# Optimization experiments

Hardware: AMD Instinct MI355X
Metric: run time of the kernel (lower is better)

Reference implementation:

```python
import jax, jax.numpy as jnp
import numpy as np

# Graph sampling geometry (2-layer neighbor sampling, fanouts 16 and 10)
N0 = 1_048_576   # layer-0 src nodes (full frontier, features supplied)
N1 = 65_536      # layer-0 dst nodes == layer-1 src nodes
N2 = 4_096       # layer-1 dst nodes (seeds)
DEG0, DEG1 = 16, 10
E0, E1 = N1 * DEG0, N2 * DEG1
D_IN, D_H, D_OUT = 128, 256, 47


def _init_linear(key, out_f, in_f):
    s = 1.0 / np.sqrt(in_f)
    return jax.random.uniform(key, (out_f, in_f), jnp.float32, -s, s)


def setup_inputs() -> dict:
    key = jax.random.key(0)
    ks = jax.random.split(key, 10)
    x = jax.random.normal(ks[0], (N0, D_IN), dtype=jnp.float32)
    # CSC: indptr over dst nodes (uniform degree), indices = src node ids
    indptr0 = jnp.arange(N1 + 1, dtype=jnp.int32) * DEG0
    indices0 = jax.random.randint(ks[1], (E0,), 0, N0, dtype=jnp.int32)
    indptr1 = jnp.arange(N2 + 1, dtype=jnp.int32) * DEG1
    indices1 = jax.random.randint(ks[2], (E1,), 0, N1, dtype=jnp.int32)
    return {
        "x": x,
        "indices0": indices0, "indptr0": indptr0,
        "indices1": indices1, "indptr1": indptr1,
        "Wl0": _init_linear(ks[3], D_H, D_IN), "bl0": jnp.zeros((D_H,), jnp.float32),
        "Wr0": _init_linear(ks[4], D_H, D_IN),
        "Wl1": _init_linear(ks[5], D_H, D_H), "bl1": jnp.zeros((D_H,), jnp.float32),
        "Wr1": _init_linear(ks[6], D_H, D_H),
        "Wo": _init_linear(ks[7], D_OUT, D_H), "bo": jnp.zeros((D_OUT,), jnp.float32),
    }


def expand_indptr(indptr, num_edges):
    # gb.expand_indptr: edge e -> dst j with indptr[j] <= e < indptr[j+1]
    e = jnp.arange(num_edges, dtype=indptr.dtype)
    return jnp.searchsorted(indptr, e, side="right") - 1


def sage_conv(h, src, dst, dst_size, Wl, bl, Wr):
    # PyG SAGEConv (mean aggr): lin_l(mean_{neighbors}) + lin_r(x_dst)
    msg = h[src]                                                    # [E, d]
    summed = jax.ops.segment_sum(msg, dst, num_segments=dst_size)  # [dst, d]
    cnt = jax.ops.segment_sum(jnp.ones_like(dst, dtype=h.dtype), dst,
                              num_segments=dst_size)
    mean = summed / jnp.maximum(cnt, 1.0)[:, None]
    return mean @ Wl.T + bl + h[:dst_size] @ Wr.T


def reference(x, indices0, indptr0, indices1, indptr1,
              Wl0, bl0, Wr0, Wl1, bl1, Wr1, Wo, bo):
    # layer 0
    dst0 = expand_indptr(indptr0, E0)
    h = sage_conv(x, indices0, dst0, N1, Wl0, bl0, Wr0)
    h = jax.nn.gelu(h, approximate=False)  # dropout p=0.0 -> identity
    # layer 1
    dst1 = expand_indptr(indptr1, E1)
    h = sage_conv(h, indices1, dst1, N2, Wl1, bl1, Wr1)
    h = jax.nn.gelu(h, approximate=False)
    # final projection
    return h @ Wo.T + bo
```

## Files before the change

kernel.cpp:

```cpp
#include <hip/hip_runtime.h>
#include <math.h>

#define N0 1048576
#define N1 65536
#define N2 4096
#define DEG0 16
#define DEG1 10
#define D_IN 128
#define D_H 256
#define D_OUT 47

__device__ __forceinline__ float gelu_exact(float x) {
    return 0.5f * x * (1.0f + erff(x * 0.70710678118654752f));
}

template <int DEG, int F4>
__global__ __launch_bounds__(256) void agg_mean_kernel(
    const float4* __restrict__ feat, const int* __restrict__ idx,
    float4* __restrict__ out, int ndst)
{
    const int lane  = threadIdx.x % F4;
    const int local = threadIdx.x / F4;
    const int per_block = 256 / F4;
    const int j = blockIdx.x * per_block + local;
    if (j >= ndst) return;

    const int* ip = idx + (long)j * DEG;
    int srcs[DEG];
#pragma unroll
    for (int e = 0; e < DEG; ++e) srcs[e] = ip[e];

    float4 acc = make_float4(0.f, 0.f, 0.f, 0.f);
#pragma unroll
    for (int e = 0; e < DEG; ++e) {
        float4 v = feat[(long)srcs[e] * F4 + lane];
        acc.x += v.x; acc.y += v.y; acc.z += v.z; acc.w += v.w;
    }
    const float r = 1.0f / (float)DEG;
    acc.x *= r; acc.y *= r; acc.z *= r; acc.w *= r;
    out[(long)j * F4 + lane] = acc;
}

template <int K1, int K2>
__global__ __launch_bounds__(256) void gemm_gelu_kernel(
    const float* __restrict__ A1, const float* __restrict__ A2,
    const float* __restrict__ B1, const float* __restrict__ B2,
    const float* __restrict__ bias, float* __restrict__ C, int M)
{
    constexpr int BM = 128, BN = 64, BK = 32;
    __shared__ float As[BK][BM + 4];
    __shared__ float Bs[BK][BN + 4];

    const int tid = threadIdx.x;
    const int bm = blockIdx.x, bn = blockIdx.y;
    const int tx = tid & 15;
    const int ty = tid >> 4;
    const int r  = tid >> 3;
    const int c4 = (tid & 7) * 4;

    float acc[8][4];
#pragma unroll
    for (int i = 0; i < 8; ++i)
#pragma unroll
        for (int j = 0; j < 4; ++j) acc[i][j] = 0.f;

    constexpr int KT = (K1 + K2) / BK;
#pragma unroll 1
    for (int kt = 0; kt < KT; ++kt) {
        const int k0 = kt * BK;
        const float* Asrc; const float* Bsrc; int koff;
        if (k0 < K1) { Asrc = A1; Bsrc = B1; koff = k0; }
        else         { Asrc = A2; Bsrc = B2; koff = k0 - K1; }
        const int lda = (k0 < K1) ? K1 : K2;

#pragma unroll
        for (int rr = 0; rr < 4; ++rr) {
            const int row = r + rr * 32;
            float4 v = *(const float4*)(Asrc + (long)(bm * BM + row) * lda + koff + c4);
            As[c4 + 0][row] = v.x; As[c4 + 1][row] = v.y;
            As[c4 + 2][row] = v.z; As[c4 + 3][row] = v.w;
        }
#pragma unroll
        for (int nn = 0; nn < 2; ++nn) {
            const int n = r + nn * 32;
            float4 v = *(const float4*)(Bsrc + (long)(bn * BN + n) * lda + koff + c4);
            Bs[c4 + 0][n] = v.x; Bs[c4 + 1][n] = v.y;
            Bs[c4 + 2][n] = v.z; Bs[c4 + 3][n] = v.w;
        }
        __syncthreads();

#pragma unroll
        for (int k = 0; k < BK; ++k) {
            float4 a0 = *(const float4*)&As[k][ty * 8];
            float4 a1 = *(const float4*)&As[k][ty * 8 + 4];
            float4 b  = *(const float4*)&Bs[k][tx * 4];
            const float av[8] = {a0.x, a0.y, a0.z, a0.w, a1.x, a1.y, a1.z, a1.w};
            const float bv[4] = {b.x, b.y, b.z, b.w};
#pragma unroll
            for (int i = 0; i < 8; ++i)
#pragma unroll
                for (int j = 0; j < 4; ++j)
                    acc[i][j] += av[i] * bv[j];
        }
        __syncthreads();
    }

    float4 b4 = *(const float4*)(bias + bn * BN + tx * 4);
    const float bb[4] = {b4.x, b4.y, b4.z, b4.w};
#pragma unroll
    for (int i = 0; i < 8; ++i) {
        const int row = bm * BM + ty * 8 + i;
        float4 o;
        o.x = gelu_exact(acc[i][0] + bb[0]);
        o.y = gelu_exact(acc[i][1] + bb[1]);
        o.z = gelu_exact(acc[i][2] + bb[2]);
        o.w = gelu_exact(acc[i][3] + bb[3]);
        *(float4*)(C + (long)row * D_H + bn * BN + tx * 4) = o;
    }
}

__global__ __launch_bounds__(64) void proj_kernel(
    const float* __restrict__ H, const float* __restrict__ Wo,
    const float* __restrict__ bo, float* __restrict__ out)
{
    __shared__ float hrow[D_H];
    const int i = blockIdx.x;
    ((float4*)hrow)[threadIdx.x] = ((const float4*)(H + (long)i * D_H))[threadIdx.x];
    __syncthreads();
    const int n = threadIdx.x;
    if (n < D_OUT) {
        const float* w = Wo + (long)n * D_H;
        float s = 0.f;
#pragma unroll 8
        for (int k = 0; k < D_H; ++k) s += hrow[k] * w[k];
        out[(long)i * D_OUT + n] = s + bo[n];
    }
}

extern "C" void kernel_launch(void* const* d_in, const int* in_sizes, int n_in,
                              void* d_out, int out_size, void* d_ws, size_t ws_size,
                              hipStream_t stream)
{
    const float* x        = (const float*)d_in[0];
    const int*   indices0 = (const int*)d_in[1];
    const int*   indices1 = (const int*)d_in[3];
    const float* Wl0 = (const float*)d_in[5];
    const float* bl0 = (const float*)d_in[6];
    const float* Wr0 = (const float*)d_in[7];
    const float* Wl1 = (const float*)d_in[8];
    const float* bl1 = (const float*)d_in[9];
    const float* Wr1 = (const float*)d_in[10];
    const float* Wo  = (const float*)d_in[11];
    const float* bo  = (const float*)d_in[12];
    float* out = (float*)d_out;

    float* mean0 = (float*)d_ws;
    float* h0    = mean0 + (size_t)N1 * D_IN;
    float* mean1 = h0    + (size_t)N1 * D_H;
    float* h1    = mean1 + (size_t)N2 * D_H;

    agg_mean_kernel<DEG0, D_IN / 4><<<N1 / (256 / (D_IN / 4)), 256, 0, stream>>>(
        (const float4*)x, indices0, (float4*)mean0, N1);

    gemm_gelu_kernel<D_IN, D_IN><<<dim3(N1 / 128, D_H / 64), 256, 0, stream>>>(
        mean0, x, Wl0, Wr0, bl0, h0, N1);

    agg_mean_kernel<DEG1, D_H / 4><<<N2 / (256 / (D_H / 4)), 256, 0, stream>>>(
        (const float4*)h0, indices1, (float4*)mean1, N2);

    gemm_gelu_kernel<D_H, D_H><<<dim3(N2 / 128, D_H / 64), 256, 0, stream>>>(
        mean1, h0, Wl1, Wr1, bl1, h1, N2);

    proj_kernel<<<N2, 64, 0, stream>>>(h1, Wo, bo, out);
}
```

Before: 869.9 us.

## Fuse aggregation with GEMM and use split-bf16 MFMA for all layers

Replaces the separate mean-aggregation and fp32 SIMT GEMM kernels with fused per-layer kernels. Each fused kernel gathers neighbor rows into registers, splits them into hi/lo bf16 pairs and runs three MFMA 16x16x32 bf16 products to keep near-fp32 accuracy. Intermediate activations are stored as bf16 hi/lo pairs, and weights are pre-split by a small prep kernel on every call. This removes the mean buffer round trips and the slow FP32 FMA GEMM. The cost is triple MFMA work and weight fragments read straight from global memory without LDS staging.

```diff
diff --git a/kernel.cpp b/kernel.cpp
--- a/kernel.cpp
+++ b/kernel.cpp
@@ -10,130 +10,311 @@
 #define D_H 256
 #define D_OUT 47
 
+typedef unsigned int uint32;
+typedef __attribute__((ext_vector_type(8))) short bf16x8;
+typedef __attribute__((ext_vector_type(4))) float f32x4;
+
+__device__ __forceinline__ unsigned short f2b(float x) {
+    uint32 u = __float_as_uint(x);
+    return (unsigned short)((u + 0x7fffu + ((u >> 16) & 1u)) >> 16);
+}
+__device__ __forceinline__ float b2f(unsigned short h) {
+    return __uint_as_float(((uint32)h) << 16);
+}
 __device__ __forceinline__ float gelu_exact(float x) {
     return 0.5f * x * (1.0f + erff(x * 0.70710678118654752f));
 }
-
-template <int DEG, int F4>
-__global__ __launch_bounds__(256) void agg_mean_kernel(
-    const float4* __restrict__ feat, const int* __restrict__ idx,
-    float4* __restrict__ out, int ndst)
-{
-    const int lane  = threadIdx.x % F4;
-    const int local = threadIdx.x / F4;
-    const int per_block = 256 / F4;
-    const int j = blockIdx.x * per_block + local;
-    if (j >= ndst) return;
-
-    const int* ip = idx + (long)j * DEG;
-    int srcs[DEG];
-#pragma unroll
-    for (int e = 0; e < DEG; ++e) srcs[e] = ip[e];
-
-    float4 acc = make_float4(0.f, 0.f, 0.f, 0.f);
-#pragma unroll
-    for (int e = 0; e < DEG; ++e) {
-        float4 v = feat[(long)srcs[e] * F4 + lane];
-        acc.x += v.x; acc.y += v.y; acc.z += v.z; acc.w += v.w;
-    }
-    const float r = 1.0f / (float)DEG;
-    acc.x *= r; acc.y *= r; acc.z *= r; acc.w *= r;
-    out[(long)j * F4 + lane] = acc;
-}
-
-template <int K1, int K2>
-__global__ __launch_bounds__(256) void gemm_gelu_kernel(
-    const float* __restrict__ A1, const float* __restrict__ A2,
-    const float* __restrict__ B1, const float* __restrict__ B2,
-    const float* __restrict__ bias, float* __restrict__ C, int M)
-{
-    constexpr int BM = 128, BN = 64, BK = 32;
-    __shared__ float As[BK][BM + 4];
-    __shared__ float Bs[BK][BN + 4];
-
-    const int tid = threadIdx.x;
-    const int bm = blockIdx.x, bn = blockIdx.y;
-    const int tx = tid & 15;
-    const int ty = tid >> 4;
-    const int r  = tid >> 3;
-    const int c4 = (tid & 7) * 4;
-
-    float acc[8][4];
-#pragma unroll
-    for (int i = 0; i < 8; ++i)
-#pragma unroll
-        for (int j = 0; j < 4; ++j) acc[i][j] = 0.f;
-
-    constexpr int KT = (K1 + K2) / BK;
-#pragma unroll 1
-    for (int kt = 0; kt < KT; ++kt) {
-        const int k0 = kt * BK;
-        const float* Asrc; const float* Bsrc; int koff;
-        if (k0 < K1) { Asrc = A1; Bsrc = B1; koff = k0; }
-        else         { Asrc = A2; Bsrc = B2; koff = k0 - K1; }
-        const int lda = (k0 < K1) ? K1 : K2;
-
-#pragma unroll
-        for (int rr = 0; rr < 4; ++rr) {
-            const int row = r + rr * 32;
-            float4 v = *(const float4*)(Asrc + (long)(bm * BM + row) * lda + koff + c4);
-            As[c4 + 0][row] = v.x; As[c4 + 1][row] = v.y;
-            As[c4 + 2][row] = v.z; As[c4 + 3][row] = v.w;
-        }
-#pragma unroll
-        for (int nn = 0; nn < 2; ++nn) {
-            const int n = r + nn * 32;
-            float4 v = *(const float4*)(Bsrc + (long)(bn * BN + n) * lda + koff + c4);
-            Bs[c4 + 0][n] = v.x; Bs[c4 + 1][n] = v.y;
-            Bs[c4 + 2][n] = v.z; Bs[c4 + 3][n] = v.w;
-        }
-        __syncthreads();
-
-#pragma unroll
-        for (int k = 0; k < BK; ++k) {
-            float4 a0 = *(const float4*)&As[k][ty * 8];
-            float4 a1 = *(const float4*)&As[k][ty * 8 + 4];
-            float4 b  = *(const float4*)&Bs[k][tx * 4];
-            const float av[8] = {a0.x, a0.y, a0.z, a0.w, a1.x, a1.y, a1.z, a1.w};
-            const float bv[4] = {b.x, b.y, b.z, b.w};
-#pragma unroll
-            for (int i = 0; i < 8; ++i)
-#pragma unroll
-                for (int j = 0; j < 4; ++j)
-                    acc[i][j] += av[i] * bv[j];
-        }
-        __syncthreads();
-    }
-
-    float4 b4 = *(const float4*)(bias + bn * BN + tx * 4);
-    const float bb[4] = {b4.x, b4.y, b4.z, b4.w};
-#pragma unroll
-    for (int i = 0; i < 8; ++i) {
-        const int row = bm * BM + ty * 8 + i;
-        float4 o;
-        o.x = gelu_exact(acc[i][0] + bb[0]);
-        o.y = gelu_exact(acc[i][1] + bb[1]);
-        o.z = gelu_exact(acc[i][2] + bb[2]);
-        o.w = gelu_exact(acc[i][3] + bb[3]);
-        *(float4*)(C + (long)row * D_H + bn * BN + tx * 4) = o;
-    }
-}
-
-__global__ __launch_bounds__(64) void proj_kernel(
-    const float* __restrict__ H, const float* __restrict__ Wo,
+__device__ __forceinline__ void split8(float4 a, float4 b, bf16x8& fh, bf16x8& fl) {
+    float t[8] = {a.x, a.y, a.z, a.w, b.x, b.y, b.z, b.w};
+#pragma unroll
+    for (int j = 0; j < 8; ++j) {
+        unsigned short h = f2b(t[j]);
+        fh[j] = (short)h;
+        fl[j] = (short)f2b(t[j] - b2f(h));
+    }
+}
+
+__global__ __launch_bounds__(256) void prep_weights(
+    const float4* __restrict__ Wl0, const float4* __restrict__ Wr0,
+    const float4* __restrict__ Wl1, const float4* __restrict__ Wr1,
+    const float4* __restrict__ Wo,
+    ushort4* __restrict__ wl0h, ushort4* __restrict__ wl0l,
+    ushort4* __restrict__ wr0h, ushort4* __restrict__ wr0l,
+    ushort4* __restrict__ wl1h, ushort4* __restrict__ wl1l,
+    ushort4* __restrict__ wr1h, ushort4* __restrict__ wr1l,
+    ushort4* __restrict__ woh,  ushort4* __restrict__ wol)
+{
+    const int b = blockIdx.x, t = threadIdx.x;
+    const float4* src; ushort4 *dh, *dl; int i, n4;
+    if (b < 32)       { src = Wl0; dh = wl0h; dl = wl0l; i = b * 256 + t;         n4 = 8192;  }
+    else if (b < 64)  { src = Wr0; dh = wr0h; dl = wr0l; i = (b - 32) * 256 + t;  n4 = 8192;  }
+    else if (b < 128) { src = Wl1; dh = wl1h; dl = wl1l; i = (b - 64) * 256 + t;  n4 = 16384; }
+    else if (b < 192) { src = Wr1; dh = wr1h; dl = wr1l; i = (b - 128) * 256 + t; n4 = 16384; }
+    else              { src = Wo;  dh = woh;  dl = wol;  i = (b - 192) * 256 + t; n4 = 3008;  }
+    if (i < n4) {
+        float4 v = src[i];
+        ushort4 h, l;
+        h.x = f2b(v.x); l.x = f2b(v.x - b2f(h.x));
+        h.y = f2b(v.y); l.y = f2b(v.y - b2f(h.y));
+        h.z = f2b(v.z); l.z = f2b(v.z - b2f(h.z));
+        h.w = f2b(v.w); l.w = f2b(v.w - b2f(h.w));
+        dh[i] = h; dl[i] = l;
+    }
+}
+
+__global__ __launch_bounds__(256) void layer0_fused(
+    const float* __restrict__ x, const int* __restrict__ idx,
+    const unsigned short* __restrict__ Blh, const unsigned short* __restrict__ Bll,
+    const unsigned short* __restrict__ Brh, const unsigned short* __restrict__ Brl,
+    const float* __restrict__ bias,
+    unsigned short* __restrict__ oh, unsigned short* __restrict__ ol)
+{
+    const int tid  = threadIdx.x;
+    const int w    = tid >> 6;
+    const int lane = tid & 63;
+    const int quad = lane >> 4;
+    const int l16  = lane & 15;
+    const int m    = blockIdx.x * 64 + w * 16 + l16;
+
+    float mean[4][8];
+#pragma unroll
+    for (int c = 0; c < 4; ++c)
+#pragma unroll
+        for (int j = 0; j < 8; ++j) mean[c][j] = 0.f;
+
+    int srcs[DEG0];
+    {
+        const int4* ip = (const int4*)(idx + (size_t)m * DEG0);
+#pragma unroll
+        for (int q = 0; q < 4; ++q) {
+            int4 v = ip[q];
+            srcs[4 * q + 0] = v.x; srcs[4 * q + 1] = v.y;
+            srcs[4 * q + 2] = v.z; srcs[4 * q + 3] = v.w;
+        }
+    }
+#pragma unroll
+    for (int e = 0; e < DEG0; ++e) {
+        const float* row = x + (size_t)srcs[e] * D_IN + quad * 8;
+#pragma unroll
+        for (int c = 0; c < 4; ++c) {
+            float4 v0 = *(const float4*)(row + c * 32);
+            float4 v1 = *(const float4*)(row + c * 32 + 4);
+            mean[c][0] += v0.x; mean[c][1] += v0.y; mean[c][2] += v0.z; mean[c][3] += v0.w;
+            mean[c][4] += v1.x; mean[c][5] += v1.y; mean[c][6] += v1.z; mean[c][7] += v1.w;
+        }
+    }
+    bf16x8 a1h[4], a1l[4];
+#pragma unroll
+    for (int c = 0; c < 4; ++c)
+#pragma unroll
+        for (int j = 0; j < 8; ++j) {
+            float v = mean[c][j] * 0.0625f;
+            unsigned short h = f2b(v);
+            a1h[c][j] = (short)h;
+            a1l[c][j] = (short)f2b(v - b2f(h));
+        }
+
+    f32x4 acc[16];
+#pragma unroll
+    for (int nt = 0; nt < 16; ++nt) acc[nt] = (f32x4)0.f;
+
+#pragma unroll
+    for (int c = 0; c < 4; ++c) {
+        const int ko = c * 32 + quad * 8;
+#pragma unroll
+        for (int nt = 0; nt < 16; ++nt) {
+            const size_t bo_ = (size_t)(nt * 16 + l16) * D_IN + ko;
+            bf16x8 bh = *(const bf16x8*)(Blh + bo_);
+            bf16x8 bl = *(const bf16x8*)(Bll + bo_);
+            acc[nt] = __builtin_amdgcn_mfma_f32_16x16x32_bf16(a1l[c], bh, acc[nt], 0, 0, 0);
+            acc[nt] = __builtin_amdgcn_mfma_f32_16x16x32_bf16(a1h[c], bl, acc[nt], 0, 0, 0);
+            acc[nt] = __builtin_amdgcn_mfma_f32_16x16x32_bf16(a1h[c], bh, acc[nt], 0, 0, 0);
+        }
+    }
+    const float* xrow = x + (size_t)m * D_IN + quad * 8;
+#pragma unroll
+    for (int c = 0; c < 4; ++c) {
+        float4 v0 = *(const float4*)(xrow + c * 32);
+        float4 v1 = *(const float4*)(xrow + c * 32 + 4);
+        bf16x8 ah, al;
+        split8(v0, v1, ah, al);
+        const int ko = c * 32 + quad * 8;
+#pragma unroll
+        for (int nt = 0; nt < 16; ++nt) {
+            const size_t bo_ = (size_t)(nt * 16 + l16) * D_IN + ko;
+            bf16x8 bh = *(const bf16x8*)(Brh + bo_);
+            bf16x8 bl = *(const bf16x8*)(Brl + bo_);
+            acc[nt] = __builtin_amdgcn_mfma_f32_16x16x32_bf16(al, bh, acc[nt], 0, 0, 0);
+            acc[nt] = __builtin_amdgcn_mfma_f32_16x16x32_bf16(ah, bl, acc[nt], 0, 0, 0);
+            acc[nt] = __builtin_amdgcn_mfma_f32_16x16x32_bf16(ah, bh, acc[nt], 0, 0, 0);
+        }
+    }
+
+    const int row0 = blockIdx.x * 64 + w * 16 + quad * 4;
+#pragma unroll
+    for (int nt = 0; nt < 16; ++nt) {
+        const int col = nt * 16 + l16;
+        const float bb = bias[col];
+#pragma unroll
+        for (int r = 0; r < 4; ++r) {
+            float v = gelu_exact(acc[nt][r] + bb);
+            unsigned short h = f2b(v);
+            const size_t o = (size_t)(row0 + r) * D_H + col;
+            oh[o] = h;
+            ol[o] = f2b(v - b2f(h));
+        }
+    }
+}
+
+__global__ __launch_bounds__(128) void layer1_fused(
+    const unsigned short* __restrict__ fh, const unsigned short* __restrict__ fl,
+    const int* __restrict__ idx,
+    const unsigned short* __restrict__ Blh, const unsigned short* __restrict__ Bll,
+    const unsigned short* __restrict__ Brh, const unsigned short* __restrict__ Brl,
+    const float* __restrict__ bias,
+    unsigned short* __restrict__ oh, unsigned short* __restrict__ ol)
+{
+    const int tid  = threadIdx.x;
+    const int w    = tid >> 6;
+    const int lane = tid & 63;
+    const int quad = lane >> 4;
+    const int l16  = lane & 15;
+    const int m    = blockIdx.x * 32 + w * 16 + l16;
+
+    float mean[8][8];
+#pragma unroll
+    for (int c = 0; c < 8; ++c)
+#pragma unroll
+        for (int j = 0; j < 8; ++j) mean[c][j] = 0.f;
+
+    int srcs[DEG1];
+#pragma unroll
+    for (int e = 0; e < DEG1; ++e) srcs[e] = idx[(size_t)m * DEG1 + e];
+
+#pragma unroll
+    for (int e = 0; e < DEG1; ++e) {
+        const unsigned short* rh = fh + (size_t)srcs[e] * D_H + quad * 8;
+        const unsigned short* rl = fl + (size_t)srcs[e] * D_H + quad * 8;
+#pragma unroll
+        for (int c = 0; c < 8; ++c) {
+            bf16x8 hv = *(const bf16x8*)(rh + c * 32);
+            bf16x8 lv = *(const bf16x8*)(rl + c * 32);
+#pragma unroll
+            for (int j = 0; j < 8; ++j)
+                mean[c][j] += b2f((unsigned short)hv[j]) + b2f((unsigned short)lv[j]);
+        }
+    }
+    bf16x8 a1h[8], a1l[8];
+#pragma unroll
+    for (int c = 0; c < 8; ++c)
+#pragma unroll
+        for (int j = 0; j < 8; ++j) {
+            float v = mean[c][j] * 0.1f;
+            unsigned short h = f2b(v);
+            a1h[c][j] = (short)h;
+            a1l[c][j] = (short)f2b(v - b2f(h));
+        }
+
+    f32x4 acc[16];
+#pragma unroll
+    for (int nt = 0; nt < 16; ++nt) acc[nt] = (f32x4)0.f;
+
+#pragma unroll
+    for (int c = 0; c < 8; ++c) {
+        const int ko = c * 32 + quad * 8;
+#pragma unroll
+        for (int nt = 0; nt < 16; ++nt) {
+            const size_t bo_ = (size_t)(nt * 16 + l16) * D_H + ko;
+            bf16x8 bh = *(const bf16x8*)(Blh + bo_);
+            bf16x8 bl = *(const bf16x8*)(Bll + bo_);
+            acc[nt] = __builtin_amdgcn_mfma_f32_16x16x32_bf16(a1l[c], bh, acc[nt], 0, 0, 0);
+            acc[nt] = __builtin_amdgcn_mfma_f32_16x16x32_bf16(a1h[c], bl, acc[nt], 0, 0, 0);
+            acc[nt] = __builtin_amdgcn_mfma_f32_16x16x32_bf16(a1h[c], bh, acc[nt], 0, 0, 0);
+        }
+    }
+    const unsigned short* arh = fh + (size_t)m * D_H + quad * 8;
+    const unsigned short* arl = fl + (size_t)m * D_H + quad * 8;
+#pragma unroll
+    for (int c = 0; c < 8; ++c) {
+        bf16x8 ah = *(const bf16x8*)(arh + c * 32);
+        bf16x8 al = *(const bf16x8*)(arl + c * 32);
+        const int ko = c * 32 + quad * 8;
+#pragma unroll
+        for (int nt = 0; nt < 16; ++nt) {
+            const size_t bo_ = (size_t)(nt * 16 + l16) * D_H + ko;
+            bf16x8 bh = *(const bf16x8*)(Brh + bo_);
+            bf16x8 bl = *(const bf16x8*)(Brl + bo_);
+            acc[nt] = __builtin_amdgcn_mfma_f32_16x16x32_bf16(al, bh, acc[nt], 0, 0, 0);
+            acc[nt] = __builtin_amdgcn_mfma_f32_16x16x32_bf16(ah, bl, acc[nt], 0, 0, 0);
+            acc[nt] = __builtin_amdgcn_mfma_f32_16x16x32_bf16(ah, bh, acc[nt], 0, 0, 0);
+        }
+    }
+
+    const int row0 = blockIdx.x * 32 + w * 16 + quad * 4;
+#pragma unroll
+    for (int nt = 0; nt < 16; ++nt) {
+        const int col = nt * 16 + l16;
+        const float bb = bias[col];
+#pragma unroll
+        for (int r = 0; r < 4; ++r) {
+            float v = gelu_exact(acc[nt][r] + bb);
+            unsigned short h = f2b(v);
+            const size_t o = (size_t)(row0 + r) * D_H + col;
+            oh[o] = h;
+            ol[o] = f2b(v - b2f(h));
+        }
+    }
+}
+
+__global__ __launch_bounds__(128) void proj_fused(
+    const unsigned short* __restrict__ fh, const unsigned short* __restrict__ fl,
+    const unsigned short* __restrict__ Wh, const unsigned short* __restrict__ Wl_,
     const float* __restrict__ bo, float* __restrict__ out)
 {
-    __shared__ float hrow[D_H];
-    const int i = blockIdx.x;
-    ((float4*)hrow)[threadIdx.x] = ((const float4*)(H + (long)i * D_H))[threadIdx.x];
-    __syncthreads();
-    const int n = threadIdx.x;
-    if (n < D_OUT) {
-        const float* w = Wo + (long)n * D_H;
-        float s = 0.f;
-#pragma unroll 8
-        for (int k = 0; k < D_H; ++k) s += hrow[k] * w[k];
-        out[(long)i * D_OUT + n] = s + bo[n];
+    const int tid  = threadIdx.x;
+    const int w    = tid >> 6;
+    const int lane = tid & 63;
+    const int quad = lane >> 4;
+    const int l16  = lane & 15;
+    const int m    = blockIdx.x * 32 + w * 16 + l16;
+
+    f32x4 acc[4];
+#pragma unroll
+    for (int nt = 0; nt < 4; ++nt) acc[nt] = (f32x4)0.f;
+
+    const unsigned short* arh = fh + (size_t)m * D_H + quad * 8;
+    const unsigned short* arl = fl + (size_t)m * D_H + quad * 8;
+#pragma unroll
+    for (int c = 0; c < 8; ++c) {
+        bf16x8 ah = *(const bf16x8*)(arh + c * 32);
+        bf16x8 al = *(const bf16x8*)(arl + c * 32);
+        const int ko = c * 32 + quad * 8;
+#pragma unroll
+        for (int nt = 0; nt < 4; ++nt) {
+            const int n = nt * 16 + l16;
+            bf16x8 bh = {0, 0, 0, 0, 0, 0, 0, 0};
+            bf16x8 bl = {0, 0, 0, 0, 0, 0, 0, 0};
+            if (n < D_OUT) {
+                const size_t o = (size_t)n * D_H + ko;
+                bh = *(const bf16x8*)(Wh + o);
+                bl = *(const bf16x8*)(Wl_ + o);
+            }
+            acc[nt] = __builtin_amdgcn_mfma_f32_16x16x32_bf16(al, bh, acc[nt], 0, 0, 0);
+            acc[nt] = __builtin_amdgcn_mfma_f32_16x16x32_bf16(ah, bl, acc[nt], 0, 0, 0);
+            acc[nt] = __builtin_amdgcn_mfma_f32_16x16x32_bf16(ah, bh, acc[nt], 0, 0, 0);
+        }
+    }
+
+    const int row0 = blockIdx.x * 32 + w * 16 + quad * 4;
+#pragma unroll
+    for (int nt = 0; nt < 4; ++nt) {
+        const int col = nt * 16 + l16;
+        if (col < D_OUT) {
+            const float bb = bo[col];
+#pragma unroll
+            for (int r = 0; r < 4; ++r)
+                out[(size_t)(row0 + r) * D_OUT + col] = acc[nt][r] + bb;
+        }
     }
 }
 
@@ -154,22 +335,35 @@
     const float* bo  = (const float*)d_in[12];
     float* out = (float*)d_out;
 
-    float* mean0 = (float*)d_ws;
-    float* h0    = mean0 + (size_t)N1 * D_IN;
-    float* mean1 = h0    + (size_t)N1 * D_H;
-    float* h1    = mean1 + (size_t)N2 * D_H;
-
-    agg_mean_kernel<DEG0, D_IN / 4><<<N1 / (256 / (D_IN / 4)), 256, 0, stream>>>(
-        (const float4*)x, indices0, (float4*)mean0, N1);
-
-    gemm_gelu_kernel<D_IN, D_IN><<<dim3(N1 / 128, D_H / 64), 256, 0, stream>>>(
-        mean0, x, Wl0, Wr0, bl0, h0, N1);
-
-    agg_mean_kernel<DEG1, D_H / 4><<<N2 / (256 / (D_H / 4)), 256, 0, stream>>>(
-        (const float4*)h0, indices1, (float4*)mean1, N2);
-
-    gemm_gelu_kernel<D_H, D_H><<<dim3(N2 / 128, D_H / 64), 256, 0, stream>>>(
-        mean1, h0, Wl1, Wr1, bl1, h1, N2);
-
-    proj_kernel<<<N2, 64, 0, stream>>>(h1, Wo, bo, out);
-}
+    unsigned short* p = (unsigned short*)d_ws;
+    unsigned short* h0h  = p; p += (size_t)N1 * D_H;
+    unsigned short* h0l  = p; p += (size_t)N1 * D_H;
+    unsigned short* h1h  = p; p += (size_t)N2 * D_H;
+    unsigned short* h1l  = p; p += (size_t)N2 * D_H;
+    unsigned short* wl0h = p; p += 256 * 128;
+    unsigned short* wl0l = p; p += 256 * 128;
+    unsigned short* wr0h = p; p += 256 * 128;
+    unsigned short* wr0l = p; p += 256 * 128;
+    unsigned short* wl1h = p; p += 256 * 256;
+    unsigned short* wl1l = p; p += 256 * 256;
+    unsigned short* wr1h = p; p += 256 * 256;
+    unsigned short* wr1l = p; p += 256 * 256;
+    unsigned short* woh  = p; p += 47 * 256;
+    unsigned short* wol  = p; p += 47 * 256;
+
+    prep_weights<<<204, 256, 0, stream>>>(
+        (const float4*)Wl0, (const float4*)Wr0, (const float4*)Wl1,
+        (const float4*)Wr1, (const float4*)Wo,
+        (ushort4*)wl0h, (ushort4*)wl0l, (ushort4*)wr0h, (ushort4*)wr0l,
+        (ushort4*)wl1h, (ushort4*)wl1l, (ushort4*)wr1h, (ushort4*)wr1l,
+        (ushort4*)woh,  (ushort4*)wol);
+
+    layer0_fused<<<N1 / 64, 256, 0, stream>>>(
+        x, indices0, wl0h, wl0l, wr0h, wr0l, bl0, h0h, h0l);
+
+    layer1_fused<<<N2 / 32, 128, 0, stream>>>(
+        h0h, h0l, indices1, wl1h, wl1l, wr1h, wr1l, bl1, h1h, h1l);
+
+    proj_fused<<<N2 / 32, 128, 0, stream>>>(
+        h1h, h1l, woh, wol, bo, out);
+}
```

Measured after the change: 957.6 us. +10.1%, slower.
